# Optimization experiments

Measured on AMD Instinct MI355X. Metric: run time of the kernel, lower is better.

The kernel has to match this reference:

```python
import jax, jax.numpy as jnp
import numpy as np

H, B, D, C = 6, 512, 2048, 1000   # heads (5 ICs + backbone exit), batch, feat dim, classes
TAU = 0.5                          # confidence_threshold


def setup_inputs() -> dict:
    key = jax.random.key(0)
    k1, k2, k3, k4 = jax.random.split(key, 4)
    feats = jax.random.normal(k1, (H, B, D), dtype=jnp.float32)          # pooled reps at each exit
    W = jax.random.normal(k2, (H, D, C), dtype=jnp.float32) * 0.07       # per-head classifier weights
    b = jax.random.normal(k3, (H, C), dtype=jnp.float32) * 0.1
    y_true = jax.random.randint(k4, (B,), 0, C)
    return {"feats": feats, "W": W, "b": b, "y_true": y_true}


def reference(feats, W, b, y_true):
    # Per-head logits for every sample (vectorized replacement for the shrinking-batch loop).
    logits = jnp.einsum('hbd,hdc->hbc', feats, W) + b[:, None, :]        # [H, B, C]
    logp = jax.nn.log_softmax(logits, axis=-1)
    conf = jnp.exp(logp).max(axis=-1)                                    # [H, B] max softmax prob (prob_conf=True)

    # Early-exit routing: first head with conf >= TAU; else head with max confidence
    # (argmax returns the first occurrence, matching the strict '>' update in find_exit).
    exited = conf >= TAU                                                  # [H, B]
    any_exit = exited.any(axis=0)                                         # [B]
    first_exit = jnp.argmax(exited, axis=0)                               # [B] first True along heads
    best_conf = jnp.argmax(conf, axis=0)                                  # [B] fallback exit
    exit_idx = jnp.where(any_exit, first_exit, best_conf)                 # [B] == sample_exited_at

    # Gather the chosen head's logits per sample (vectorized masked-scatter of sample_outputs).
    outputs = jnp.take_along_axis(logits, exit_idx[None, :, None], axis=0)[0]   # [B, C]

    # criterion_ic: cross-entropy loss + accuracy on routed outputs
    out_logp = jax.nn.log_softmax(outputs, axis=-1)
    loss = -jnp.take_along_axis(out_logp, y_true[:, None], axis=1).mean()
    acc = (outputs.argmax(axis=-1) == y_true).astype(jnp.float32).mean()
    return outputs, exit_idx.astype(jnp.int32), loss, acc
```

## Files before the change

kernel.cpp:

```cpp
#include <hip/hip_runtime.h>
#include <hip/hip_bf16.h>
#include <math.h>

#define Hn 6
#define Bn 512
#define Dn 2048
#define Cn 1000
#define Cpad 1024
#define TAUv 0.5f
#define KSPLIT 4
#define KPER (Dn / KSPLIT)
#define NIT (KPER / 32)

typedef unsigned int u32;
typedef unsigned short u16;
typedef __attribute__((ext_vector_type(8))) short short8;
typedef __attribute__((ext_vector_type(4))) float f32x4;

union FragU { u32 d[4]; short8 s; };

__device__ __forceinline__ u32 cvt_pk2(float f0, float f1) {
  union { __hip_bfloat162 h; u32 u; } cv;
  cv.h = __float22bfloat162_rn(make_float2(f0, f1));
  return cv.u;
}

__device__ __forceinline__ void pack8f(const float* f, FragU& hi, FragU& lo) {
  float r[8];
#pragma unroll
  for (int i = 0; i < 4; ++i) {
    const u32 d = cvt_pk2(f[2 * i], f[2 * i + 1]);
    hi.d[i] = d;
    r[2 * i]     = f[2 * i]     - __uint_as_float(d << 16);
    r[2 * i + 1] = f[2 * i + 1] - __uint_as_float(d & 0xffff0000u);
  }
#pragma unroll
  for (int i = 0; i < 4; ++i) lo.d[i] = cvt_pk2(r[2 * i], r[2 * i + 1]);
}

__device__ __forceinline__ void dma16(const void* g, void* l) {
  __builtin_amdgcn_global_load_lds(
      (const __attribute__((address_space(1))) u32*)g,
      (__attribute__((address_space(3))) u32*)l, 16, 0, 0);
}

__global__ __launch_bounds__(256, 2) void gemm_k(
    const float* __restrict__ feats, const float* __restrict__ W,
    const float* __restrict__ bias, float* __restrict__ logits,
    float* __restrict__ scalars)
{
  const int h  = blockIdx.z >> 2;
  const int kz = blockIdx.z & 3;
  const int m0 = blockIdx.y * 128;
  const int n0 = blockIdx.x * 128;
  const int t = threadIdx.x, lane = t & 63, w = t >> 6;

  if (t == 0 && blockIdx.x == 0 && blockIdx.y == 0 && blockIdx.z == 0) {
    scalars[0] = 0.f; scalars[1] = 0.f;
  }

  __shared__ __align__(16) float lds[2][8192];

  const float* gsrc; size_t gci, gadv; int dst0;
  if (w < 2) {
    const int r = w * 64 + (lane >> 3);
    const int q = (lane & 7) ^ ((lane >> 3) & 7);
    gsrc = feats + ((size_t)(h * Bn + m0 + r)) * Dn + kz * KPER + q * 4;
    gci  = (size_t)8 * Dn;
    gadv = 32;
    dst0 = w * 8192 + lane * 16;
  } else {
    const int kk  = (w - 2) * 16 + (lane >> 5);
    const int c4  = n0 + (lane & 31) * 4;
    const int c4c = (c4 + 3 < Cn) ? c4 : (Cn - 4);
    gsrc = W + ((size_t)h * Dn + kz * KPER + kk) * Cn + c4c;
    gci  = (size_t)2 * Cn;
    gadv = (size_t)32 * Cn;
    dst0 = 16384 + (w - 2) * 8192 + lane * 16;
  }

  const int fl = lane & 15, fq = lane >> 4;
  const int wm = (w & 1) * 64, wn = (w >> 1) * 64;
  const int sxor = fl & 7;

  f32x4 acc[4][4];
#pragma unroll
  for (int i = 0; i < 4; ++i)
#pragma unroll
    for (int j = 0; j < 4; ++j) acc[i][j] = (f32x4){0.f, 0.f, 0.f, 0.f};

  {
    char* sb = (char*)&lds[0][0];
#pragma unroll
    for (int i = 0; i < 8; ++i) dma16(gsrc + i * gci, sb + dst0 + i * 1024);
  }
  __syncthreads();

#define COMPUTE_TILE(IT)                                                              \
  {                                                                                   \
    const char*  ab = (const char*)&lds[(IT) & 1][0];                                 \
    const float* bb = (const float*)(ab + 16384);                                     \
    FragU ah[4], al[4];                                                               \
    _Pragma("unroll")                                                                 \
    for (int mt = 0; mt < 4; ++mt) {                                                  \
      const int r = wm + mt * 16 + fl;                                                \
      const float4 v0 = *(const float4*)(ab + r * 128 + ((((fq * 2)    ) ^ sxor) * 16)); \
      const float4 v1 = *(const float4*)(ab + r * 128 + ((((fq * 2) + 1) ^ sxor) * 16)); \
      float f[8] = {v0.x, v0.y, v0.z, v0.w, v1.x, v1.y, v1.z, v1.w};                  \
      pack8f(f, ah[mt], al[mt]);                                                      \
    }                                                                                 \
    _Pragma("unroll")                                                                 \
    for (int nt = 0; nt < 4; ++nt) {                                                  \
      const int n = wn + nt * 16 + fl;                                                \
      float f[8];                                                                     \
      _Pragma("unroll")                                                               \
      for (int e = 0; e < 8; ++e) f[e] = bb[(fq * 8 + e) * 128 + n];                  \
      FragU bh, bl;                                                                   \
      pack8f(f, bh, bl);                                                              \
      _Pragma("unroll")                                                               \
      for (int mt = 0; mt < 4; ++mt) {                                                \
        acc[mt][nt] = __builtin_amdgcn_mfma_f32_16x16x32_bf16(ah[mt].s, bh.s, acc[mt][nt], 0, 0, 0); \
        acc[mt][nt] = __builtin_amdgcn_mfma_f32_16x16x32_bf16(ah[mt].s, bl.s, acc[mt][nt], 0, 0, 0); \
        acc[mt][nt] = __builtin_amdgcn_mfma_f32_16x16x32_bf16(al[mt].s, bh.s, acc[mt][nt], 0, 0, 0); \
      }                                                                               \
    }                                                                                 \
  }

  for (int it = 0; it < NIT - 1; ++it) {
    char* sb = (char*)&lds[(it + 1) & 1][0];
    const float* g = gsrc + (size_t)(it + 1) * gadv;
#pragma unroll
    for (int i = 0; i < 8; ++i) dma16(g + i * gci, sb + dst0 + i * 1024);
    COMPUTE_TILE(it);
    __syncthreads();
  }
  COMPUTE_TILE(NIT - 1);
#undef COMPUTE_TILE

  float* part = logits + (size_t)kz * ((size_t)Hn * Bn * Cn);
#pragma unroll
  for (int nt = 0; nt < 4; ++nt) {
    const int col = n0 + wn + nt * 16 + fl;
    if (col >= Cn) continue;
    const float bv = (kz == 0) ? bias[(size_t)h * Cn + col] : 0.f;
#pragma unroll
    for (int mt = 0; mt < 4; ++mt) {
      const int rbase = m0 + wm + mt * 16 + fq * 4;
#pragma unroll
      for (int r = 0; r < 4; ++r)
        part[((size_t)h * Bn + rbase + r) * Cn + col] = acc[mt][nt][r] + bv;
    }
  }
}

__global__ __launch_bounds__(256) void confpick_k(
    const float* __restrict__ logits, const int* __restrict__ y,
    float* __restrict__ out, float* __restrict__ out_exit,
    float* __restrict__ scalars)
{
  const int b = blockIdx.x, tid = threadIdx.x;
  const int lane = tid & 63, w = tid >> 6;
  const size_t S = (size_t)Hn * Bn * Cn;
  __shared__ float ms[Hn], ss[Hn];

  for (int h = w; h < Hn; h += 4) {
    const float* p = logits + ((size_t)h * Bn + b) * Cn;
    float vv[16];
#pragma unroll
    for (int i = 0; i < 4; ++i) {
      const int c4 = i * 256 + lane * 4;
      if (c4 + 3 < Cn) {
        const float4 v0 = *(const float4*)(p + c4);
        const float4 v1 = *(const float4*)(p + S + c4);
        const float4 v2 = *(const float4*)(p + 2 * S + c4);
        const float4 v3 = *(const float4*)(p + 3 * S + c4);
        vv[4 * i + 0] = v0.x + v1.x + v2.x + v3.x;
        vv[4 * i + 1] = v0.y + v1.y + v2.y + v3.y;
        vv[4 * i + 2] = v0.z + v1.z + v2.z + v3.z;
        vv[4 * i + 3] = v0.w + v1.w + v2.w + v3.w;
      } else {
#pragma unroll
        for (int j = 0; j < 4; ++j) {
          const int c = c4 + j;
          vv[4 * i + j] = (c < Cn) ? p[c] + p[S + c] + p[2 * S + c] + p[3 * S + c]
                                   : -3.4e38f;
        }
      }
    }
    float m = -3.4e38f;
#pragma unroll
    for (int i = 0; i < 16; ++i) m = fmaxf(m, vv[i]);
#pragma unroll
    for (int off = 32; off >= 1; off >>= 1) m = fmaxf(m, __shfl_xor(m, off));
    float s = 0.f;
#pragma unroll
    for (int i = 0; i < 16; ++i) s += (vv[i] > -3.0e38f) ? expf(vv[i] - m) : 0.f;
#pragma unroll
    for (int off = 32; off >= 1; off >>= 1) s += __shfl_xor(s, off);
    if (lane == 0) { ms[h] = m; ss[h] = s; }
  }
  __syncthreads();

  int first = -1, best = 0;
  float bestc = -3.4e38f;
#pragma unroll
  for (int h = 0; h < Hn; ++h) {
    const float c = 1.0f / ss[h];
    if (first < 0 && c >= TAUv) first = h;
    if (c > bestc) { bestc = c; best = h; }
  }
  const int ex = (first >= 0) ? first : best;
  const float* p = logits + ((size_t)ex * Bn + b) * Cn;

  const int c4 = tid * 4;
  float vv[4] = {-3.4e38f, -3.4e38f, -3.4e38f, -3.4e38f};
  if (c4 + 3 < Cn) {
    const float4 v0 = *(const float4*)(p + c4);
    const float4 v1 = *(const float4*)(p + S + c4);
    const float4 v2 = *(const float4*)(p + 2 * S + c4);
    const float4 v3 = *(const float4*)(p + 3 * S + c4);
    vv[0] = v0.x + v1.x + v2.x + v3.x;
    vv[1] = v0.y + v1.y + v2.y + v3.y;
    vv[2] = v0.z + v1.z + v2.z + v3.z;
    vv[3] = v0.w + v1.w + v2.w + v3.w;
  }
  float vm = -3.4e38f; int im = 1 << 30;
#pragma unroll
  for (int j = 0; j < 4; ++j) {
    const int c = c4 + j;
    if (c < Cn) {
      out[(size_t)b * Cn + c] = vv[j];
      if (vv[j] > vm) { vm = vv[j]; im = c; }
    }
  }
#pragma unroll
  for (int off = 32; off >= 1; off >>= 1) {
    const float ov = __shfl_xor(vm, off);
    const int   oi = __shfl_xor(im, off);
    if (ov > vm || (ov == vm && oi < im)) { vm = ov; im = oi; }
  }
  __shared__ float rm[4]; __shared__ int ri[4];
  if (lane == 0) { rm[w] = vm; ri[w] = im; }
  __syncthreads();
  if (tid == 0) {
    float bm = rm[0]; int bi = ri[0];
    for (int q = 1; q < 4; ++q)
      if (rm[q] > bm || (rm[q] == bm && ri[q] < bi)) { bm = rm[q]; bi = ri[q]; }
    const int yt = y[b];
    const float ryt = p[yt] + p[S + yt] + p[2 * S + yt] + p[3 * S + yt];
    const float lp = ryt - ms[ex] - logf(ss[ex]);
    out_exit[b] = (float)ex;
    atomicAdd(&scalars[0], -lp * (1.0f / (float)Bn));
    atomicAdd(&scalars[1], ((bi == yt) ? 1.f : 0.f) * (1.0f / (float)Bn));
  }
}

extern "C" void kernel_launch(void* const* d_in, const int* in_sizes, int n_in,
                              void* d_out, int out_size, void* d_ws, size_t ws_size,
                              hipStream_t stream) {
  const float* feats = (const float*)d_in[0];
  const float* W     = (const float*)d_in[1];
  const float* bias  = (const float*)d_in[2];
  const int*   y     = (const int*)d_in[3];
  float* out = (float*)d_out;

  float* logits = (float*)d_ws;
  float* out_exit    = out + (size_t)Bn * Cn;
  float* out_scalars = out + (size_t)Bn * Cn + Bn;

  gemm_k<<<dim3(Cpad / 128, Bn / 128, Hn * KSPLIT), 256, 0, stream>>>(
      feats, W, bias, logits, out_scalars);
  confpick_k<<<Bn, 256, 0, stream>>>(logits, y, out, out_exit, out_scalars);
}
```

Before: 191.8 us.

## Overlap next-tile DMA with compute via partial vmcnt waits and swizzle W tile

Rewrites the GEMM main loop so the next tile's global-to-LDS loads stay in flight while the current tile is computed. Each iteration waits with vmcnt(8) on only the older batch of loads, where the previous __syncthreads forced every load to finish. It also XOR-swizzles the column placement of the W tile in LDS, with matching read addresses, to reduce bank conflicts on the column-strided B-fragment reads. The risk is relying on the hand-written waitcnt and barrier ordering being correct for the asynchronous LDS loads.

```diff
diff --git a/kernel.cpp b/kernel.cpp
--- a/kernel.cpp
+++ b/kernel.cpp
@@ -61,23 +61,15 @@
 
   __shared__ __align__(16) float lds[2][8192];
 
-  const float* gsrc; size_t gci, gadv; int dst0;
-  if (w < 2) {
-    const int r = w * 64 + (lane >> 3);
-    const int q = (lane & 7) ^ ((lane >> 3) & 7);
-    gsrc = feats + ((size_t)(h * Bn + m0 + r)) * Dn + kz * KPER + q * 4;
-    gci  = (size_t)8 * Dn;
-    gadv = 32;
-    dst0 = w * 8192 + lane * 16;
-  } else {
-    const int kk  = (w - 2) * 16 + (lane >> 5);
-    const int c4  = n0 + (lane & 31) * 4;
-    const int c4c = (c4 + 3 < Cn) ? c4 : (Cn - 4);
-    gsrc = W + ((size_t)h * Dn + kz * KPER + kk) * Cn + c4c;
-    gci  = (size_t)2 * Cn;
-    gadv = (size_t)32 * Cn;
-    dst0 = 16384 + (w - 2) * 8192 + lane * 16;
-  }
+  const int rA = (w & 1) * 64 + (lane >> 3);
+  const int qA = (lane & 7) ^ ((lane >> 3) & 7);
+  const float* gsrcA = feats + ((size_t)(h * Bn + m0 + rA)) * Dn + kz * KPER + qA * 4;
+  const size_t gciA = (size_t)8 * Dn;
+  const int dstA = w * 8192 + lane * 16;
+  const int kb = (w - 2) * 16 + (lane >> 5);
+  const int pB = lane & 31;
+  const float* Wrow = W + ((size_t)h * Dn + kz * KPER) * Cn;
+  const int dstB = 16384 + (w - 2) * 8192 + lane * 16;
 
   const int fl = lane & 15, fq = lane >> 4;
   const int wm = (w & 1) * 64, wn = (w >> 1) * 64;
@@ -89,12 +81,25 @@
 #pragma unroll
     for (int j = 0; j < 4; ++j) acc[i][j] = (f32x4){0.f, 0.f, 0.f, 0.f};
 
-  {
-    char* sb = (char*)&lds[0][0];
-#pragma unroll
-    for (int i = 0; i < 8; ++i) dma16(gsrc + i * gci, sb + dst0 + i * 1024);
-  }
-  __syncthreads();
+#define STAGE(TILE)                                                                   \
+  {                                                                                   \
+    char* sb = (char*)&lds[(TILE) & 1][0];                                            \
+    if (w < 2) {                                                                      \
+      const float* g = gsrcA + (size_t)(TILE) * 32;                                   \
+      _Pragma("unroll")                                                               \
+      for (int i = 0; i < 8; ++i) dma16(g + i * gciA, sb + dstA + i * 1024);          \
+    } else {                                                                          \
+      const size_t kt0 = (size_t)(TILE) * 32;                                         \
+      _Pragma("unroll")                                                               \
+      for (int i = 0; i < 8; ++i) {                                                   \
+        const int kl = kb + 2 * i;                                                    \
+        const int pc = pB ^ (((kl >> 3) & 3) << 2);                                   \
+        int col = n0 + pc * 4;                                                        \
+        col = (col + 3 < Cn) ? col : (Cn - 4);                                        \
+        dma16(Wrow + (kt0 + kl) * Cn + col, sb + dstB + i * 1024);                    \
+      }                                                                               \
+    }                                                                                 \
+  }
 
 #define COMPUTE_TILE(IT)                                                              \
   {                                                                                   \
@@ -112,9 +117,10 @@
     _Pragma("unroll")                                                                 \
     for (int nt = 0; nt < 4; ++nt) {                                                  \
       const int n = wn + nt * 16 + fl;                                                \
+      const int nsw = ((((n >> 2) ^ (fq << 2)) << 2) | (n & 3));                      \
       float f[8];                                                                     \
       _Pragma("unroll")                                                               \
-      for (int e = 0; e < 8; ++e) f[e] = bb[(fq * 8 + e) * 128 + n];                  \
+      for (int e = 0; e < 8; ++e) f[e] = bb[(fq * 8 + e) * 128 + nsw];                \
       FragU bh, bl;                                                                   \
       pack8f(f, bh, bl);                                                              \
       _Pragma("unroll")                                                               \
@@ -126,16 +132,24 @@
     }                                                                                 \
   }
 
+  STAGE(0);
+
   for (int it = 0; it < NIT - 1; ++it) {
-    char* sb = (char*)&lds[(it + 1) & 1][0];
-    const float* g = gsrc + (size_t)(it + 1) * gadv;
-#pragma unroll
-    for (int i = 0; i < 8; ++i) dma16(g + i * gci, sb + dst0 + i * 1024);
+    STAGE(it + 1);
+    asm volatile("s_waitcnt vmcnt(8)" ::: "memory");
+    __builtin_amdgcn_s_barrier();
+    __builtin_amdgcn_sched_barrier(0);
     COMPUTE_TILE(it);
-    __syncthreads();
-  }
+    __builtin_amdgcn_sched_barrier(0);
+    asm volatile("s_waitcnt lgkmcnt(0)" ::: "memory");
+    __builtin_amdgcn_s_barrier();
+  }
+  asm volatile("s_waitcnt vmcnt(0)" ::: "memory");
+  __builtin_amdgcn_s_barrier();
+  __builtin_amdgcn_sched_barrier(0);
   COMPUTE_TILE(NIT - 1);
 #undef COMPUTE_TILE
+#undef STAGE
 
   float* part = logits + (size_t)kz * ((size_t)Hn * Bn * Cn);
 #pragma unroll
```

Result: no change. 188.9 us (-1.5%).
